# Kernel optimization log

Measured on AMD Instinct MI355X. Metric: run time of the kernel, lower is better.

Reference implementation:

```python
import jax, jax.numpy as jnp
import numpy as np

N_NODES = 100000
N_EDGES = 1600000
IN_DIM = 29
OUT_DIM = 64
BN_EPS = 1e-5


def setup_inputs() -> dict:
    key = jax.random.key(0)
    k1, k2, k3, k4, k5, k6, k7, k8 = jax.random.split(key, 8)
    node = jax.random.normal(k1, (N_NODES, 3), dtype=jnp.float32)
    features = jax.random.normal(k2, (N_NODES, IN_DIM), dtype=jnp.float32)
    edges = jax.random.randint(k3, (N_EDGES, 2), 0, N_NODES, dtype=jnp.int64)
    # Linear(input_dim+3, output_dim, bias=False): weight [out, in+3]
    fan_in = IN_DIM + 3
    weight = jax.random.uniform(k4, (OUT_DIM, fan_in), dtype=jnp.float32,
                                minval=-1.0, maxval=1.0) / np.sqrt(fan_in)
    # BatchNorm1d(output_dim) in eval mode: affine params + running stats
    gamma = jax.random.normal(k5, (OUT_DIM,), dtype=jnp.float32) * 0.1 + 1.0
    beta = jax.random.normal(k6, (OUT_DIM,), dtype=jnp.float32) * 0.1
    running_mean = jax.random.normal(k7, (OUT_DIM,), dtype=jnp.float32) * 0.1
    running_var = jax.random.uniform(k8, (OUT_DIM,), dtype=jnp.float32,
                                     minval=0.5, maxval=1.5)
    return {"node": node, "features": features, "edges": edges,
            "weight": weight, "gamma": gamma, "beta": beta,
            "running_mean": running_mean, "running_var": running_var}


def reference(node, features, edges, weight, gamma, beta, running_mean, running_var):
    dst = edges[:, 0]  # pos_i index (pooling destination)
    src = edges[:, 1]  # pos_j / x_j index
    # gather + concat: msg [E, in+3]
    msg = jnp.concatenate([features[src], node[src] - node[dst]], axis=1)
    # Linear (no bias): [E, out]
    msg = jnp.einsum('ei,oi->eo', msg, weight)
    # BatchNorm1d (eval mode, running stats)
    inv_std = gamma / jnp.sqrt(running_var + BN_EPS)
    msg = (msg - running_mean) * inv_std + beta
    # scatter-max pooling over destination nodes (fixed N segments;
    # torch.unique + scatter_reduce(amax) == segment_max restricted to covered
    # nodes; empty segments filled with 0 matching the zeros init)
    pooled = jax.ops.segment_max(msg, dst, num_segments=N_NODES)
    return jnp.where(jnp.isneginf(pooled), 0.0, pooled)
```

## Files before the change

kernel.cpp:

```cpp
#include <hip/hip_runtime.h>
#include <hip/hip_fp16.h>

#define IN_DIM 29
#define XDIM 32
#define OUT_DIM 64
#define BN_EPS 1e-5f

#define BW      32
#define BW_LOG  5
#define TNODES  64
#define MAXBUCK 4096
#define SENT    0


__global__ __launch_bounds__(256) void fused_tc_kernel(
    const float* __restrict__ features, const float* __restrict__ node,
    const float* __restrict__ weight, const float* __restrict__ gamma,
    const float* __restrict__ rvar, unsigned short* __restrict__ yq,
    const int* __restrict__ edges, int* __restrict__ gHist,
    int n_nodes, int n_edges, int nbuck, int chunk, int nblk)
{
    __shared__ __align__(16) int smem[MAXBUCK];
    if ((int)blockIdx.x < nblk) {
        int* h = smem;
        for (int i = threadIdx.x; i < nbuck; i += 256) h[i] = 0;
        __syncthreads();
        const int e0 = blockIdx.x * chunk;
        const int e1 = min(e0 + chunk, n_edges);
        const int2* ep = (const int2*)edges;
        for (int e = e0 + threadIdx.x; e < e1; e += 256)
            atomicAdd(&h[ep[e].x >> BW_LOG], 1);
        __syncthreads();
        for (int i = threadIdx.x; i < nbuck; i += 256)
            gHist[i * nblk + blockIdx.x] = h[i];
    } else {
        float* stage = (float*)smem;
        const int tid  = threadIdx.x;
        const int lane = tid & 63, wid = tid >> 6;
        const int n0   = ((int)blockIdx.x - nblk) * TNODES;
        const int nrem = min(TNODES, n_nodes - n0);

        for (int idx = tid; idx < nrem * XDIM; idx += 256) {
            const int r = idx >> 5, c = idx & 31;
            float v = (c < IN_DIM) ? features[(size_t)(n0 + r) * IN_DIM + c]
                                   : node[(size_t)(n0 + r) * 3 + (c - IN_DIM)];
            stage[idx] = v;
        }

        const float a = gamma[lane] * __frsqrt_rn(rvar[lane] + BN_EPS);
        float w[XDIM];
        const float4* wp = (const float4*)(weight + lane * XDIM);
#pragma unroll
        for (int q = 0; q < 8; ++q) {
            float4 v = wp[q];
            w[4*q+0] = v.x * a; w[4*q+1] = v.y * a;
            w[4*q+2] = v.z * a; w[4*q+3] = v.w * a;
        }
        __syncthreads();

        const int r0 = wid * (TNODES / 4);
        const int r1 = min(r0 + TNODES / 4, nrem);
        for (int r = r0; r < r1; ++r) {
            const float4* xs = (const float4*)(stage + r * XDIM);
            float a0 = 0.f, a1 = 0.f, a2 = 0.f, a3 = 0.f;
#pragma unroll
            for (int q = 0; q < 8; ++q) {
                float4 x = xs[q];
                a0 = fmaf(x.x, w[4*q+0], a0);
                a1 = fmaf(x.y, w[4*q+1], a1);
                a2 = fmaf(x.z, w[4*q+2], a2);
                a3 = fmaf(x.w, w[4*q+3], a3);
            }
            const float acc = (a0 + a1) + (a2 + a3);
            unsigned short hh = __half_as_ushort(__float2half(acc));
            unsigned short enc = (hh & 0x8000) ? (unsigned short)(~hh)
                                               : (unsigned short)(hh | 0x8000);
            yq[(size_t)(n0 + r) * OUT_DIM + lane] = enc;
        }
    }
}

__global__ __launch_bounds__(256) void scan_a_kernel(
    int* __restrict__ data, int n, int* __restrict__ aux)
{
    const int t = threadIdx.x;
    const int base = blockIdx.x * 1024 + t * 4;
    int v[4];
#pragma unroll
    for (int k = 0; k < 4; ++k) v[k] = (base + k < n) ? data[base + k] : 0;
    int tsum = v[0] + v[1] + v[2] + v[3];

    const int lane = t & 63, wv = t >> 6;
    int x = tsum;
#pragma unroll
    for (int off = 1; off < 64; off <<= 1) {
        int y = __shfl_up(x, off);
        if (lane >= off) x += y;
    }
    __shared__ int wsum[4];
    if (lane == 63) wsum[wv] = x;
    __syncthreads();
    int wexcl = 0;
    for (int i = 0; i < wv; ++i) wexcl += wsum[i];
    int run = wexcl + x - tsum;
#pragma unroll
    for (int k = 0; k < 4; ++k) {
        if (base + k < n) data[base + k] = run;
        run += v[k];
    }
    if (t == 255) aux[blockIdx.x] = run;
}

__global__ __launch_bounds__(256) void scan_b_kernel(int* __restrict__ aux, int nb) {
    const int t = threadIdx.x;
    const int lane = t & 63, wv = t >> 6;
    __shared__ int wsum[4];
    __shared__ int s_run;
    if (t == 0) s_run = 0;
    __syncthreads();
    for (int base = 0; base < nb; base += 256) {
        const int i = base + t;
        int v = (i < nb) ? aux[i] : 0;
        int x = v;
#pragma unroll
        for (int off = 1; off < 64; off <<= 1) {
            int y = __shfl_up(x, off);
            if (lane >= off) x += y;
        }
        if (lane == 63) wsum[wv] = x;
        __syncthreads();
        int wexcl = 0;
        for (int k = 0; k < wv; ++k) wexcl += wsum[k];
        const int run = s_run;
        if (i < nb) aux[i] = run + wexcl + x - v;
        __syncthreads();
        if (t == 255) s_run = run + wexcl + x;
        __syncthreads();
    }
}

__global__ __launch_bounds__(512) void partition_kernel(
    const int* __restrict__ edges, const int* __restrict__ gOffs,
    const int* __restrict__ aux,
    int* __restrict__ keys, int n_edges, int nbuck, int chunk, int nblk)
{
    __shared__ int cur[MAXBUCK];
    for (int i = threadIdx.x; i < nbuck; i += 512) {
        const int idx = i * nblk + blockIdx.x;
        cur[i] = gOffs[idx] + aux[idx >> 10];
    }
    __syncthreads();
    const int e0 = blockIdx.x * chunk;
    const int e1 = min(e0 + chunk, n_edges);
    for (int e = e0 + threadIdx.x; e < e1; e += 512) {
        const int dst = edges[2*e], src = edges[2*e+1];
        const int b = dst >> BW_LOG;
        const int pos = atomicAdd(&cur[b], 1);
        keys[pos] = (dst & (BW - 1)) | (src << BW_LOG);
    }
}

__global__ __launch_bounds__(256) void pool_fused_kernel(
    const int* __restrict__ gOffs, const int* __restrict__ aux,
    const int* __restrict__ keys,
    const unsigned short* __restrict__ yq, const float* __restrict__ node,
    const float* __restrict__ weight, const float* __restrict__ gamma,
    const float* __restrict__ beta, const float* __restrict__ rmean,
    const float* __restrict__ rvar,
    float* __restrict__ out, int n_nodes, int n_edges, int nbuck, int nblk)
{
    __shared__ int acc[BW * OUT_DIM];
    const int tid = threadIdx.x;
    const int lane = tid & 63, wid = tid >> 6;
    const int b = blockIdx.x;

    {
        int4* p = (int4*)acc;
        for (int i = tid; i < BW * OUT_DIM / 4; i += 256)
            p[i] = make_int4(SENT, SENT, SENT, SENT);
    }
    __syncthreads();

    const int i0 = b * nblk;
    const int beg = gOffs[i0] + aux[i0 >> 10];
    int end;
    if (b == nbuck - 1) end = n_edges;
    else {
        const int i1 = (b + 1) * nblk;
        end = gOffs[i1] + aux[i1 >> 10];
    }

    const int cnt = end - beg;
    const int slice = (cnt + 3) >> 2;
    const int w_beg = beg + wid * slice;
    const int w_end = min(w_beg + slice, end);

    if (w_beg < w_end) {
        const int last = w_end - 1;
        int j = w_beg;
        int kv = keys[min(j + lane, last)];
        while (j < w_end) {
            const int jn = j + 64;
            int kv_n = 0;
            if (jn < w_end) kv_n = keys[min(jn + lane, last)];
            const int m = w_end - j < 64 ? w_end - j : 64;
            const int ng = (m + 7) >> 3;

            unsigned int va[8]; int da[8];
#pragma unroll
            for (int u = 0; u < 8; ++u) {
                const int uu = (u < m) ? u : (m - 1);
                const int key = __builtin_amdgcn_readlane(kv, uu);
                da[u] = key & (BW - 1);
                va[u] = yq[(size_t)((unsigned)key >> BW_LOG) * OUT_DIM + lane];
            }
            for (int g = 0; g < ng; ++g) {
                unsigned int vb[8]; int db[8];
                const bool more = (g + 1 < ng);
                if (more) {
#pragma unroll
                    for (int u = 0; u < 8; ++u) {
                        int uu = (g + 1) * 8 + u; uu = (uu < m) ? uu : (m - 1);
                        const int key = __builtin_amdgcn_readlane(kv, uu);
                        db[u] = key & (BW - 1);
                        vb[u] = yq[(size_t)((unsigned)key >> BW_LOG) * OUT_DIM + lane];
                    }
                }
#pragma unroll
                for (int u = 0; u < 8; ++u)
                    atomicMax(&acc[da[u] * OUT_DIM + lane], (int)va[u]);
                if (more) {
#pragma unroll
                    for (int u = 0; u < 8; ++u) { va[u] = vb[u]; da[u] = db[u]; }
                }
            }
            j = jn; kv = kv_n;
        }
    }
    __syncthreads();

    const float a  = gamma[lane] * __frsqrt_rn(rvar[lane] + BN_EPS);
    const float bp = beta[lane] - rmean[lane] * a;
    const float w29 = weight[lane * XDIM + 29] * a;
    const float w30 = weight[lane * XDIM + 30] * a;
    const float w31 = weight[lane * XDIM + 31] * a;

    for (int d = wid; d < BW; d += 4) {
        const int dg = b * BW + d;
        if (dg >= n_nodes) break;
        const int k = acc[d * OUT_DIM + lane];
        float rr;
        if (k == SENT) {
            rr = 0.0f;
        } else {
            const unsigned short enc = (unsigned short)k;
            const unsigned short h = (enc & 0x8000) ? (unsigned short)(enc ^ 0x8000)
                                                    : (unsigned short)(~enc);
            const float v = __half2float(__ushort_as_half(h));
            const float nx = node[(size_t)dg * 3 + 0];
            const float ny = node[(size_t)dg * 3 + 1];
            const float nz = node[(size_t)dg * 3 + 2];
            rr = v + (bp - (w29 * nx + w30 * ny + w31 * nz));
        }
        out[(size_t)dg * OUT_DIM + lane] = rr;
    }
}

__global__ void init_kernel(int4* __restrict__ out, int total4) {
    int t = blockIdx.x * blockDim.x + threadIdx.x;
    if (t < total4) out[t] = make_int4(INT_MIN, INT_MIN, INT_MIN, INT_MIN);
}

__global__ __launch_bounds__(256) void edge_atomic_kernel(
    const int* __restrict__ edges,
    const float* __restrict__ features, const float* __restrict__ node,
    const float* __restrict__ weight, const float* __restrict__ gamma,
    const float* __restrict__ beta, const float* __restrict__ rmean,
    const float* __restrict__ rvar,
    int* __restrict__ out, int n_edges, int epw)
{
    const int lane = threadIdx.x & 63;
    const int wave = (blockIdx.x * blockDim.x + threadIdx.x) >> 6;
    int e0 = wave * epw, e1 = e0 + epw;
    if (e1 > n_edges) e1 = n_edges;

    float w[XDIM];
    const float4* wp = (const float4*)(weight + lane * XDIM);
#pragma unroll
    for (int q = 0; q < 8; ++q) {
        float4 v = wp[q];
        w[4*q+0] = v.x; w[4*q+1] = v.y; w[4*q+2] = v.z; w[4*q+3] = v.w;
    }
    const float a = gamma[lane] * __frsqrt_rn(rvar[lane] + BN_EPS);
    const float bprime = beta[lane] - rmean[lane] * a;

    for (int e = e0; e < e1; ++e) {
        const int dst = edges[2*e+0], src = edges[2*e+1];
        float x[XDIM];
#pragma unroll
        for (int i = 0; i < IN_DIM; ++i) x[i] = features[(size_t)src * IN_DIM + i];
#pragma unroll
        for (int j = 0; j < 3; ++j)
            x[IN_DIM+j] = node[(size_t)src*3+j] - node[(size_t)dst*3+j];
        float acc = 0.0f;
#pragma unroll
        for (int i = 0; i < XDIM; ++i) acc = fmaf(x[i], w[i], acc);
        float msg = fmaf(acc, a, bprime);
        int bb = __float_as_int(msg);
        int key = (bb < 0) ? (bb ^ 0x7FFFFFFF) : bb;
        atomicMax(out + (size_t)dst * OUT_DIM + lane, key);
    }
}

__global__ void decode_kernel(int* __restrict__ out, int total) {
    int t = blockIdx.x * blockDim.x + threadIdx.x;
    if (t >= total) return;
    int k = out[t];
    float r;
    if (k == INT_MIN) r = 0.0f;
    else { int b = (k < 0) ? (k ^ 0x7FFFFFFF) : k; r = __int_as_float(b); }
    ((float*)out)[t] = r;
}

extern "C" void kernel_launch(void* const* d_in, const int* in_sizes, int n_in,
                              void* d_out, int out_size, void* d_ws, size_t ws_size,
                              hipStream_t stream) {
    const float* node     = (const float*)d_in[0];
    const float* features = (const float*)d_in[1];
    const int*   edges    = (const int*)d_in[2];
    const float* weight   = (const float*)d_in[3];
    const float* gamma    = (const float*)d_in[4];
    const float* beta     = (const float*)d_in[5];
    const float* rmean    = (const float*)d_in[6];
    const float* rvar     = (const float*)d_in[7];

    const int n_nodes = in_sizes[0] / 3;
    const int n_edges = in_sizes[2] / 2;

    const int nbuck = (n_nodes + BW - 1) >> BW_LOG;

    int nblk = 0; size_t o_yq=0, o_hist=0, o_aux=0, o_keys=0; size_t need = 0;
    for (int cand = 128; cand >= 32; cand >>= 1) {
        const int n_scan = nbuck * cand;
        const int nb_scan = (n_scan + 1023) / 1024;
        size_t off = 0;
        auto alloc = [&](size_t bytes) { size_t r = off; off = (off + bytes + 15) & ~(size_t)15; return r; };
        o_yq   = alloc((size_t)n_nodes * OUT_DIM * sizeof(unsigned short));
        o_hist = alloc((size_t)n_scan * sizeof(int));
        o_aux  = alloc((size_t)nb_scan * sizeof(int));
        o_keys = alloc((size_t)n_edges * sizeof(int));
        need = off;
        if (need <= ws_size) { nblk = cand; break; }
    }

    if (nblk > 0 && nbuck <= MAXBUCK && n_nodes <= MAXBUCK * BW) {
        const int n_scan = nbuck * nblk;
        const int nb_scan = (n_scan + 1023) / 1024;
        const int chunk = (n_edges + nblk - 1) / nblk;
        const int ntb = (n_nodes + TNODES - 1) / TNODES;

        char* base  = (char*)d_ws;
        unsigned short* yq = (unsigned short*)(base + o_yq);
        int* gHist  = (int*)(base + o_hist);
        int* aux    = (int*)(base + o_aux);
        int* keys   = (int*)(base + o_keys);

        fused_tc_kernel<<<nblk + ntb, 256, 0, stream>>>(
            features, node, weight, gamma, rvar, yq,
            edges, gHist, n_nodes, n_edges, nbuck, chunk, nblk);
        scan_a_kernel<<<nb_scan, 256, 0, stream>>>(gHist, n_scan, aux);
        scan_b_kernel<<<1, 256, 0, stream>>>(aux, nb_scan);
        partition_kernel<<<nblk, 512, 0, stream>>>(edges, gHist, aux, keys,
                                                   n_edges, nbuck, chunk, nblk);
        pool_fused_kernel<<<nbuck, 256, 0, stream>>>(
            gHist, aux, keys, yq, node, weight, gamma, beta, rmean, rvar,
            (float*)d_out, n_nodes, n_edges, nbuck, nblk);
    } else {
        int* out_i = (int*)d_out;
        const int total4 = out_size / 4;
        init_kernel<<<(total4 + 255) / 256, 256, 0, stream>>>((int4*)out_i, total4);
        const int n_waves = 8192;
        const int epw = (n_edges + n_waves - 1) / n_waves;
        edge_atomic_kernel<<<n_waves / 4, 256, 0, stream>>>(
            edges, features, node, weight, gamma, beta, rmean, rvar,
            out_i, n_edges, epw);
        decode_kernel<<<(out_size + 255) / 256, 256, 0, stream>>>(out_i, out_size);
    }
}
```

Measured before the change: 181.5 us.

## Vectorize edge reads, raise partition block count, widen pool kernel to 8 waves

The histogram and partition kernels now read two edges at once as an int4 load, with a scalar tail for an odd remainder. The per-block chunk is rounded to an even count so those loads stay 16-byte aligned. The host now tries up to 512 partition blocks, which spreads partitioning across more CUs but makes the histogram and scan arrays four times larger. The pool kernel moves to 512 threads, with 8 waves splitting each bucket's edges, to raise per-bucket parallelism and occupancy for the shared-memory atomicMax phase.

```diff
diff --git a/kernel.cpp b/kernel.cpp
--- a/kernel.cpp
+++ b/kernel.cpp
@@ -27,9 +27,15 @@
         __syncthreads();
         const int e0 = blockIdx.x * chunk;
         const int e1 = min(e0 + chunk, n_edges);
-        const int2* ep = (const int2*)edges;
-        for (int e = e0 + threadIdx.x; e < e1; e += 256)
-            atomicAdd(&h[ep[e].x >> BW_LOG], 1);
+        const int np = (e1 - e0) >> 1;
+        const int4* ep4 = (const int4*)(edges + 2 * e0);
+        for (int p = threadIdx.x; p < np; p += 256) {
+            int4 v = ep4[p];
+            atomicAdd(&h[v.x >> BW_LOG], 1);
+            atomicAdd(&h[v.z >> BW_LOG], 1);
+        }
+        if (((e1 - e0) & 1) && threadIdx.x == 0)
+            atomicAdd(&h[edges[2 * (e1 - 1)] >> BW_LOG], 1);
         __syncthreads();
         for (int i = threadIdx.x; i < nbuck; i += 256)
             gHist[i * nblk + blockIdx.x] = h[i];
@@ -152,15 +158,26 @@
     __syncthreads();
     const int e0 = blockIdx.x * chunk;
     const int e1 = min(e0 + chunk, n_edges);
-    for (int e = e0 + threadIdx.x; e < e1; e += 512) {
-        const int dst = edges[2*e], src = edges[2*e+1];
+    const int np = (e1 - e0) >> 1;
+    const int4* ep4 = (const int4*)(edges + 2 * e0);
+    for (int p = threadIdx.x; p < np; p += 512) {
+        int4 v = ep4[p];
+        const int b0 = v.x >> BW_LOG;
+        const int p0 = atomicAdd(&cur[b0], 1);
+        keys[p0] = (v.x & (BW - 1)) | (v.y << BW_LOG);
+        const int b1 = v.z >> BW_LOG;
+        const int p1 = atomicAdd(&cur[b1], 1);
+        keys[p1] = (v.z & (BW - 1)) | (v.w << BW_LOG);
+    }
+    if (((e1 - e0) & 1) && threadIdx.x == 0) {
+        const int dst = edges[2 * (e1 - 1)], src = edges[2 * (e1 - 1) + 1];
         const int b = dst >> BW_LOG;
         const int pos = atomicAdd(&cur[b], 1);
         keys[pos] = (dst & (BW - 1)) | (src << BW_LOG);
     }
 }
 
-__global__ __launch_bounds__(256) void pool_fused_kernel(
+__global__ __launch_bounds__(512) void pool_fused_kernel(
     const int* __restrict__ gOffs, const int* __restrict__ aux,
     const int* __restrict__ keys,
     const unsigned short* __restrict__ yq, const float* __restrict__ node,
@@ -176,7 +193,7 @@
 
     {
         int4* p = (int4*)acc;
-        for (int i = tid; i < BW * OUT_DIM / 4; i += 256)
+        for (int i = tid; i < BW * OUT_DIM / 4; i += 512)
             p[i] = make_int4(SENT, SENT, SENT, SENT);
     }
     __syncthreads();
@@ -191,7 +208,7 @@
     }
 
     const int cnt = end - beg;
-    const int slice = (cnt + 3) >> 2;
+    const int slice = (cnt + 7) >> 3;
     const int w_beg = beg + wid * slice;
     const int w_end = min(w_beg + slice, end);
 
@@ -245,7 +262,7 @@
     const float w30 = weight[lane * XDIM + 30] * a;
     const float w31 = weight[lane * XDIM + 31] * a;
 
-    for (int d = wid; d < BW; d += 4) {
+    for (int d = wid; d < BW; d += 8) {
         const int dg = b * BW + d;
         if (dg >= n_nodes) break;
         const int k = acc[d * OUT_DIM + lane];
@@ -340,7 +357,7 @@
     const int nbuck = (n_nodes + BW - 1) >> BW_LOG;
 
     int nblk = 0; size_t o_yq=0, o_hist=0, o_aux=0, o_keys=0; size_t need = 0;
-    for (int cand = 128; cand >= 32; cand >>= 1) {
+    for (int cand = 512; cand >= 32; cand >>= 1) {
         const int n_scan = nbuck * cand;
         const int nb_scan = (n_scan + 1023) / 1024;
         size_t off = 0;
@@ -356,7 +373,8 @@
     if (nblk > 0 && nbuck <= MAXBUCK && n_nodes <= MAXBUCK * BW) {
         const int n_scan = nbuck * nblk;
         const int nb_scan = (n_scan + 1023) / 1024;
-        const int chunk = (n_edges + nblk - 1) / nblk;
+        int chunk = (n_edges + nblk - 1) / nblk;
+        chunk = (chunk + 1) & ~1;
         const int ntb = (n_nodes + TNODES - 1) / TNODES;
 
         char* base  = (char*)d_ws;
@@ -372,7 +390,7 @@
         scan_b_kernel<<<1, 256, 0, stream>>>(aux, nb_scan);
         partition_kernel<<<nblk, 512, 0, stream>>>(edges, gHist, aux, keys,
                                                    n_edges, nbuck, chunk, nblk);
-        pool_fused_kernel<<<nbuck, 256, 0, stream>>>(
+        pool_fused_kernel<<<nbuck, 512, 0, stream>>>(
             gHist, aux, keys, yq, node, weight, gamma, beta, rmean, rvar,
             (float*)d_out, n_nodes, n_edges, nbuck, nblk);
     } else {
```

Measured after the change: 196.7 us. +8.4%, slower.
